# Kernel tuning notes

Hardware: AMD Instinct MI355X
Metric: run time of the kernel (lower is better)

The kernel has to match this reference:

```python
import jax, jax.numpy as jnp
import numpy as np
from jax import lax

E, C, N = 3, 2, 2048          # edge types, channels, nodes (= nb_items)
B, T = 64, 50                 # batch, max_seq_length
W_IN = 256; W_OUT = 256; U = 512  # gcn in/out, rnn_units


def setup_inputs() -> dict:
    key = jax.random.key(0)
    ks = jax.random.split(key, 16)
    # sparse-ish adjacency stored densely (coalesce/spspmm equivalents are dense ops)
    A = jnp.where(jax.random.uniform(ks[0], (E, N, N)) < 0.01,
                  jax.random.uniform(ks[1], (E, N, N)), 0.0)
    X = jax.random.normal(ks[2], (N, W_IN)) * 0.1
    seqs = (jax.random.uniform(ks[3], (B, T, N)) < 0.005).astype(jnp.float32)  # multi-hot baskets
    seq_len = jax.random.randint(ks[4], (B,), 1, T + 1)
    h0 = jnp.zeros((B, U), jnp.float32)
    c0 = jnp.zeros((B, U), jnp.float32)
    # GTConv weights: init constant 1 (softmax -> uniform filter)
    gt_w1 = jnp.ones((C, E), jnp.float32)
    gt_w2 = jnp.ones((C, E), jnp.float32)
    gt_w3 = jnp.ones((C, E), jnp.float32)
    s_in = 1.0 / np.sqrt(W_IN)
    gcn_W = jax.random.normal(ks[5], (W_IN, W_OUT)) * s_in
    gcn_b = jnp.zeros((W_OUT,), jnp.float32)
    lin1_W = jax.random.normal(ks[6], (C * W_OUT, W_OUT)) * (1.0 / np.sqrt(C * W_OUT))
    lin1_b = jnp.zeros((W_OUT,), jnp.float32)
    s_u = 1.0 / np.sqrt(U)
    lstm_Wih = jax.random.normal(ks[7], (4 * U, W_OUT)) * s_u
    lstm_Whh = jax.random.normal(ks[8], (4 * U, U)) * s_u
    lstm_bih = jnp.zeros((4 * U,), jnp.float32)
    lstm_bhh = jnp.zeros((4 * U,), jnp.float32)
    score_W = jax.random.normal(ks[9], (N, U)) * s_u
    return {"A": A, "X": X, "seqs": seqs, "seq_len": seq_len, "h0": h0, "c0": c0,
            "gt_w1": gt_w1, "gt_w2": gt_w2, "gt_w3": gt_w3,
            "gcn_W": gcn_W, "gcn_b": gcn_b, "lin1_W": lin1_W, "lin1_b": lin1_b,
            "lstm_Wih": lstm_Wih, "lstm_Whh": lstm_Whh,
            "lstm_bih": lstm_bih, "lstm_bhh": lstm_bhh, "score_W": score_W}


def _gtconv(A, w):
    # filter = softmax over edge types; per-channel convex combine of adjacencies
    f = jax.nn.softmax(w, axis=1)            # [C,E]
    return jnp.einsum('ce,enm->cnm', f, A)   # [C,N,N]


def _col_normalize(H):
    # remove self loops; deg = scatter_add over col; value *= deg_col^-1 (no_grad deg)
    H = H * (1.0 - jnp.eye(N, dtype=H.dtype))
    deg = H.sum(axis=1)                      # [C,N] per-column degree
    dinv = lax.stop_gradient(jnp.where(deg > 0, 1.0 / deg, 0.0))
    return H * dinv[:, None, :]


def _gcn(M, X, W, b):
    # PyG GCNConv: add self loops, sym-normalize by col/row degree, aggregate at target
    M1 = M + jnp.eye(N, dtype=M.dtype)
    deg = M1.sum(axis=0)                     # scatter over col
    dis = jnp.where(deg > 0, lax.rsqrt(deg), 0.0)
    Ahat = dis[:, None] * M1 * dis[None, :]
    return Ahat.T @ (X @ W) + b              # out[target] = sum_src norm * x[src]


def reference(A, X, seqs, seq_len, h0, c0, gt_w1, gt_w2, gt_w3,
              gcn_W, gcn_b, lin1_W, lin1_b,
              lstm_Wih, lstm_Whh, lstm_bih, lstm_bhh, score_W):
    # --- GT layers: H = conv1(A) @ conv2(A), then H = norm(H) @ conv(A) ---
    HA = _gtconv(A, gt_w1)
    HB = _gtconv(A, gt_w2)
    H = jnp.einsum('cnk,ckm->cnm', HA, HB)          # spspmm per channel
    Hn = _col_normalize(H)
    HB2 = _gtconv(A, gt_w3)
    H = jnp.einsum('cnk,ckm->cnm', Hn, HB2)
    # --- GCN per channel, relu, concat, linear1 ---
    feats = [jax.nn.relu(_gcn(H[i], X, gcn_W, gcn_b)) for i in range(C)]
    X_ = jnp.concatenate(feats, axis=1) @ lin1_W + lin1_b   # [N, W_OUT]
    # --- basket max-pooling over items in each basket (empty -> zeros) ---
    def pool_step(_, mask_t):                # mask_t: [B,N]
        masked = jnp.where(mask_t[:, :, None] > 0, X_[None, :, :], -jnp.inf)
        pooled = masked.max(axis=1)          # [B, W_OUT]
        has = mask_t.sum(axis=1) > 0
        return None, jnp.where(has[:, None], pooled, 0.0)
    _, bs = lax.scan(pool_step, None, jnp.swapaxes(seqs, 0, 1))  # [T,B,W_OUT]
    # --- single-layer LSTM (PyTorch gate order i,f,g,o) ---
    def lstm_step(carry, x_t):
        h, c = carry
        g = x_t @ lstm_Wih.T + h @ lstm_Whh.T + lstm_bih + lstm_bhh
        i, f, gg, o = jnp.split(g, 4, axis=-1)
        c = jax.nn.sigmoid(f) * c + jax.nn.sigmoid(i) * jnp.tanh(gg)
        h = jax.nn.sigmoid(o) * jnp.tanh(c)
        return (h, c), h
    _, outs = lax.scan(lstm_step, (h0, c0), bs)      # [T,B,U]
    lstm_out = jnp.swapaxes(outs, 0, 1)              # [B,T,U]
    actual = lstm_out[jnp.arange(B), seq_len - 1]    # [B,U] last valid step
    return jax.nn.sigmoid(actual @ score_W.T)        # [B,N]
```

## Files before the change

kernel.cpp:

```cpp
#include <hip/hip_runtime.h>
#include <stdint.h>

#define E_ 3
#define C_ 2
#define N_ 2048
#define B_ 64
#define T_ 50
#define WIN_ 256
#define WOUT_ 256
#define U_ 512
#define BT_ (B_*T_)
#define BTP_ 3328

typedef unsigned short u16;
typedef unsigned int u32;
typedef __bf16 bf16x8 __attribute__((ext_vector_type(8)));
typedef float f32x4 __attribute__((ext_vector_type(4)));

#define NN_ (2048LL*2048LL)

__device__ __forceinline__ float bf2f(u16 u){
  u32 x = ((u32)u) << 16; return __builtin_bit_cast(float, x);
}
__device__ __forceinline__ u16 f2bf(float f){
  u32 x = __builtin_bit_cast(u32, f);
  u32 r = (x + 0x7fffu + ((x >> 16) & 1u)) >> 16;
  return (u16)r;
}

__device__ __forceinline__ void gload16(const u16* g, u16* l){
  __builtin_amdgcn_global_load_lds((const __attribute__((address_space(1))) u32*)g,
                                   (__attribute__((address_space(3))) u32*)l, 16, 0, 0);
}

__global__ void k_prep0(const float* __restrict__ w1, const float* __restrict__ w2,
                        const float* __restrict__ w3, float* __restrict__ filt,
                        const float* __restrict__ bih, const float* __restrict__ bhh,
                        float* __restrict__ bsum, u32* __restrict__ flagv){
  const int i = blockIdx.x*256 + threadIdx.x;
  bsum[i] = bih[i] + bhh[i];
  flagv[i] = 0;
  if(blockIdx.x==0 && threadIdx.x < 3*C_){
    const int t = threadIdx.x;
    const int fi = t / C_, c = t % C_;
    const float* w = (fi==0) ? w1 : ((fi==1) ? w2 : w3);
    float v[E_]; float mx = -3.4e38f;
    for(int e=0;e<E_;e++){ v[e] = w[c*E_+e]; mx = fmaxf(mx, v[e]); }
    float s = 0.f;
    for(int e=0;e<E_;e++){ v[e] = expf(v[e]-mx); s += v[e]; }
    for(int e=0;e<E_;e++) filt[(fi*C_+c)*E_ + e] = v[e]/s;
  }
}

__global__ void k_combineAll(const float* __restrict__ A, const float* __restrict__ filt,
                             u16* __restrict__ HA, u16* __restrict__ HBt){
  __shared__ float te[3][32][33];
  const int ti = blockIdx.x, tj = blockIdx.y;
  const int x = threadIdx.x, y0 = threadIdx.y;
  #pragma unroll
  for(int i=0;i<4;i++){
    const int y = y0 + i*8;
    const long base = (long)(tj*32+y)*N_ + ti*32 + x;
    const float a0 = A[0*NN_+base], a1 = A[1*NN_+base], a2 = A[2*NN_+base];
    te[0][y][x]=a0; te[1][y][x]=a1; te[2][y][x]=a2;
    #pragma unroll
    for(int c=0;c<C_;c++)
      HA[c*NN_ + base] = f2bf(filt[c*E_]*a0 + filt[c*E_+1]*a1 + filt[c*E_+2]*a2);
  }
  __syncthreads();
  #pragma unroll
  for(int i=0;i<4;i++){
    const int y = y0 + i*8;
    const long ob = (long)(ti*32+y)*N_ + tj*32 + x;
    const float a0=te[0][x][y], a1=te[1][x][y], a2=te[2][x][y];
    #pragma unroll
    for(int c=0;c<C_;c++)
      HBt[c*NN_+ob] = f2bf(filt[(C_+c)*E_]*a0 + filt[(C_+c)*E_+1]*a1 + filt[(C_+c)*E_+2]*a2);
  }
}

__global__ void k_combineT2(const float* __restrict__ A, const float* __restrict__ f,
                            u16* __restrict__ outp){
  __shared__ float te[3][32][33];
  const int ti = blockIdx.x, tj = blockIdx.y;
  const int x = threadIdx.x, y0 = threadIdx.y;
  #pragma unroll
  for(int i=0;i<4;i++){
    const int y = y0 + i*8;
    const long base = (long)(tj*32+y)*N_ + ti*32 + x;
    te[0][y][x]=A[0*NN_+base]; te[1][y][x]=A[1*NN_+base]; te[2][y][x]=A[2*NN_+base];
  }
  __syncthreads();
  #pragma unroll
  for(int i=0;i<4;i++){
    const int y = y0 + i*8;
    const long ob = (long)(ti*32+y)*N_ + tj*32 + x;
    const float a0=te[0][x][y], a1=te[1][x][y], a2=te[2][x][y];
    #pragma unroll
    for(int c=0;c<C_;c++)
      outp[c*NN_+ob] = f2bf(f[c*E_]*a0 + f[c*E_+1]*a1 + f[c*E_+2]*a2);
  }
}

template<int MODE>
__global__ __launch_bounds__(256) void gemm_bt(
    const u16* __restrict__ Ag, const u16* __restrict__ Bg, void* __restrict__ Cg,
    int K, int ldc, long sA, long sB, long sC,
    const float* __restrict__ disv, int sDis, const float* __restrict__ bias)
{
  __shared__ u16 At[128*32];
  __shared__ u16 Bt[128*32];
  const int tid = threadIdx.x;
  const int w = tid >> 6, l = tid & 63;
  const int z = blockIdx.z;
  const u16* Ab = Ag + (long)z*sA;
  const u16* Bb = Bg + (long)z*sB;
  const int rowBase = blockIdx.y*128;
  const int colBase = blockIdx.x*128;

  f32x4 acc[4][4];
  #pragma unroll
  for(int i=0;i<4;i++)
    #pragma unroll
    for(int j=0;j<4;j++)
      acc[i][j] = f32x4{0.f,0.f,0.f,0.f};

  const int wr = w >> 1, wc = w & 1;
  const int arow0 = (w*2+0)*16 + (l>>2);
  const int arow1 = (w*2+1)*16 + (l>>2);
  const int kc = (((l&3) ^ ((l>>2)&3)))*8;
  const int frow = l & 15;
  const int fkc = l >> 4;

  const int nk = K >> 5;
  for(int kt=0; kt<nk; ++kt){
    const int k0 = kt << 5;
    gload16(Ab + (long)(rowBase+arow0)*K + k0 + kc, &At[(w*2+0)*512]);
    gload16(Ab + (long)(rowBase+arow1)*K + k0 + kc, &At[(w*2+1)*512]);
    gload16(Bb + (long)(colBase+arow0)*K + k0 + kc, &Bt[(w*2+0)*512]);
    gload16(Bb + (long)(colBase+arow1)*K + k0 + kc, &Bt[(w*2+1)*512]);
    __syncthreads();
    bf16x8 af[4], bfv[4];
    #pragma unroll
    for(int m=0;m<4;m++){
      const int rr = wr*64 + m*16 + frow;
      af[m] = *(const bf16x8*)&At[rr*32 + ((fkc ^ (rr&3))<<3)];
    }
    #pragma unroll
    for(int n=0;n<4;n++){
      const int rr = wc*64 + n*16 + frow;
      bfv[n] = *(const bf16x8*)&Bt[rr*32 + ((fkc ^ (rr&3))<<3)];
    }
    #pragma unroll
    for(int m=0;m<4;m++)
      #pragma unroll
      for(int n=0;n<4;n++)
        acc[m][n] = __builtin_amdgcn_mfma_f32_16x16x32_bf16(af[m], bfv[n], acc[m][n], 0, 0, 0);
    __syncthreads();
  }

  #pragma unroll
  for(int m=0;m<4;m++){
    const int row0 = rowBase + wr*64 + m*16 + (l>>4)*4;
    #pragma unroll
    for(int n=0;n<4;n++){
      const int col = colBase + wc*64 + n*16 + (l&15);
      #pragma unroll
      for(int r=0;r<4;r++){
        const float v = acc[m][n][r];
        if(MODE==1){
          ((u16*)Cg)[z*sC + (long)(row0+r)*ldc + col] = f2bf(v);
        } else if(MODE==2){
          float o = disv[z*(long)sDis + row0 + r]*v + bias[col];
          o = o > 0.f ? o : 0.f;
          ((u16*)Cg)[z*sC + (long)(row0+r)*ldc + col] = f2bf(o);
        } else if(MODE==3){
          ((float*)Cg)[z*sC + (long)(row0+r)*ldc + col] = v + bias[col];
        } else if(MODE==4){
          const int row = row0 + r;
          if(row < BT_){
            const int bb = row/50, tt = row - bb*50;
            const int gq = col >> 9, ugg = col & 511;
            ((float*)Cg)[((((long)tt*4 + (bb>>4))*512 + ugg)*16 + (bb&15))*4 + gq] = v + bias[col];
          }
        }
      }
    }
  }
}

__global__ void k_degpart(const u16* __restrict__ H, float* __restrict__ partial){
  const int c = blockIdx.z;
  const int col = blockIdx.x*256 + threadIdx.x;
  const int r0 = blockIdx.y*128;
  const u16* Hc = H + c*NN_;
  float s = 0.f;
  #pragma unroll 4
  for(int r=0;r<128;r++) s += bf2f(Hc[(long)(r0+r)*N_ + col]);
  partial[((long)c*16 + blockIdx.y)*N_ + col] = s;
}

__global__ void k_dinv(const u16* __restrict__ H, const float* __restrict__ partial,
                       float* __restrict__ dinvb){
  const int i = blockIdx.x*256 + threadIdx.x;
  const int c = i >> 11, m = i & (N_-1);
  float s = 0.f;
  #pragma unroll
  for(int p=0;p<16;p++) s += partial[((long)c*16 + p)*N_ + m];
  s -= bf2f(H[c*NN_ + (long)m*N_ + m]);
  dinvb[i] = s > 0.f ? 1.f/s : 0.f;
}

__global__ void k_colscale(u16* __restrict__ H, const float* __restrict__ dinvb){
  const long i = (long)blockIdx.x*256 + threadIdx.x;
  const int c = blockIdx.y;
  const int j = (int)(i >> 11), ii = (int)(i & (N_-1));
  const long idx = c*NN_ + i;
  const float v = (j==ii) ? 0.f : bf2f(H[idx])*dinvb[c*N_ + ii];
  H[idx] = f2bf(v);
}

__global__ void k_gcnprep(const u16* __restrict__ H2t, float* __restrict__ disv){
  const int c = blockIdx.y, j = blockIdx.x;
  const u16* r = H2t + (c*(long)N_ + j)*N_;
  float s = 0.f;
  for(int i=threadIdx.x;i<N_;i+=256) s += bf2f(r[i]);
  __shared__ float red[256];
  red[threadIdx.x] = s;
  __syncthreads();
  for(int st=128; st>0; st>>=1){
    if(threadIdx.x < st) red[threadIdx.x] += red[threadIdx.x+st];
    __syncthreads();
  }
  if(threadIdx.x==0){
    const float deg = red[0] + 1.f;
    disv[c*N_ + j] = deg > 0.f ? rsqrtf(deg) : 0.f;
  }
}

__global__ void k_pd(const u16* __restrict__ H2t, const float* __restrict__ disv,
                     u16* __restrict__ Pd){
  const long i = (long)blockIdx.x*256 + threadIdx.x;
  const int c = blockIdx.y;
  const int j = (int)(i >> 11);
  const int ii = (int)(i & (N_-1));
  const long idx = c*NN_ + i;
  const float v = bf2f(H2t[idx]) + (ii==j ? 1.f : 0.f);
  Pd[idx] = f2bf(v*disv[c*N_ + ii]);
}

__global__ void k_transpose3(const float* __restrict__ gcnW, u16* __restrict__ Wt,
                             const float* __restrict__ lin1W, u16* __restrict__ l1Wt,
                             const float* __restrict__ scoreW, u16* __restrict__ sWt){
  const float* in; u16* out; int R, Cc;
  if(blockIdx.z==0){ in=gcnW;  out=Wt;   R=WIN_;     Cc=WOUT_; }
  else if(blockIdx.z==1){ in=lin1W; out=l1Wt; R=C_*WOUT_; Cc=WOUT_; }
  else { in=scoreW; out=sWt; R=N_; Cc=U_; }
  const int ti = blockIdx.x, tj = blockIdx.y;
  if(ti >= (Cc>>5) || tj >= (R>>5)) return;
  __shared__ float tt[32][33];
  const int x = threadIdx.x, y0 = threadIdx.y;
  #pragma unroll
  for(int i=0;i<4;i++){
    const int y = y0 + i*8;
    tt[y][x] = in[(long)(tj*32+y)*Cc + ti*32 + x];
  }
  __syncthreads();
  #pragma unroll
  for(int i=0;i<4;i++){
    const int y = y0 + i*8;
    out[(long)(ti*32+y)*R + tj*32 + x] = f2bf(tt[x][y]);
  }
}

__global__ void k_cast2(const float* __restrict__ X, u16* __restrict__ Xbf,
                        const float* __restrict__ Wih, u16* __restrict__ Wihbf){
  const long i = (long)blockIdx.x*256 + threadIdx.x;
  if(i < (long)N_*WIN_) Xbf[i] = f2bf(X[i]);
  else { const long j = i - (long)N_*WIN_; Wihbf[j] = f2bf(Wih[j]); }
}

__global__ void k_pool(const float* __restrict__ seqs, const float* __restrict__ X_,
                       u16* __restrict__ bs){
  const int t = blockIdx.x, b = blockIdx.y;
  const int f = threadIdx.x;
  if(t >= T_){
    bs[(long)(BT_ + b*2 + (t-T_))*WOUT_ + f] = 0;
    return;
  }
  const float* mask = seqs + ((long)b*T_ + t)*N_;
  __shared__ int list[N_];
  __shared__ int cnt;
  if(f==0) cnt = 0;
  __syncthreads();
  for(int n0=f; n0<N_; n0+=256){
    if(mask[n0] > 0.f){
      int p = atomicAdd(&cnt, 1);
      list[p] = n0;
    }
  }
  __syncthreads();
  const int m = cnt;
  float mx = -3.4e38f;
  for(int i=0;i<m;i++)
    mx = fmaxf(mx, X_[(long)list[i]*WOUT_ + f]);
  bs[((long)b*T_ + t)*WOUT_ + f] = f2bf(m>0 ? mx : 0.f);
}

__global__ void k_packWhh3(const float* __restrict__ Whh, u16* __restrict__ P){
  const long idx = (long)blockIdx.x*256 + threadIdx.x;
  const int e  = (int)(idx & 7);
  const int kk = (int)((idx >> 3) & 15);
  const int l  = (int)((idx >> 7) & 63);
  const int w  = (int)((idx >> 13) & 7);
  const int s  = (int)(idx >> 16);
  const int lr = w*16 + (l & 15);
  const int gam = lr & 3, ui = lr >> 2;
  const int grow = gam*512 + s*32 + ui;
  const int k = kk*32 + (l >> 4)*8 + e;
  P[idx] = f2bf(Whh[(long)grow*512 + k]);
}

__global__ void k_hinit(const float* __restrict__ h0, u16* __restrict__ Hglob){
  const int idx = blockIdx.x*256 + threadIdx.x;
  const int b = idx >> 9, u = idx & 511;
  const int grp = b >> 4, bl = b & 15;
  Hglob[grp*16384 + (bl << 9) + (u ^ ((bl & 7) << 3))] = f2bf(h0[idx]);
}

__global__ __launch_bounds__(512) void k_lstm_all(
    const u16* __restrict__ WhhP, const float* __restrict__ Gq,
    const float* __restrict__ c0v, const int* __restrict__ seqlen,
    u16* __restrict__ Hglob, u32* __restrict__ flagv, float* __restrict__ act)
{
  __shared__ u16 Hl[16*512];
  const int tid = threadIdx.x;
  const int w = tid >> 6, l = tid & 63;
  const int grp = blockIdx.x & 3, s = blockIdx.x >> 2;
  const int fr = l & 15, hi = l >> 4;

  bf16x8 wreg[16];
  const u16* wp = WhhP + (((long)s*8 + w)*64 + l)*128;
  #pragma unroll
  for(int kk=0; kk<16; ++kk)
    wreg[kk] = *(const bf16x8*)&wp[kk*8];

  const int ui = w*4 + hi;
  const int ug = s*32 + ui;
  const int bl = fr;
  const int bg = grp*16 + bl;
  float cst = c0v[bg*U_ + ug];
  const int sl = seqlen[bg] - 1;
  u16* Hbase = Hglob + grp*16384;
  const int hswz = (bl & 7) << 3;
  const int fi = (grp*16 + fr)*32;
  const long gqbase = (((long)grp*512 + ug)*16 + bl)*4;

  float4 gq_nxt = *(const float4*)&Gq[gqbase];

  for(int t=0; t<T_; ++t){
    const float4 gq = gq_nxt;
    const u16* Hin = Hbase + (t & 1)*8192;
    #pragma unroll
    for(int r=0; r<2; ++r)
      gload16(Hin + (r*8 + w)*512 + l*8, &Hl[(r*8 + w)*512]);
    __syncthreads();

    f32x4 acc = f32x4{0.f,0.f,0.f,0.f};
    #pragma unroll
    for(int kk=0; kk<16; ++kk){
      const int ke = kk*32 + hi*8;
      bf16x8 bb = *(const bf16x8*)&Hl[(bl << 9) + (ke ^ hswz)];
      acc = __builtin_amdgcn_mfma_f32_16x16x32_bf16(wreg[kk], bb, acc, 0, 0, 0);
    }

    if(t+1 < T_)
      gq_nxt = *(const float4*)&Gq[(long)(t+1)*(4*2048*16) + gqbase];

    const float a0 = acc[0] + gq.x;
    const float a1 = acc[1] + gq.y;
    const float a2 = acc[2] + gq.z;
    const float a3 = acc[3] + gq.w;
    const float ig = 1.f/(1.f + expf(-a0));
    const float fg = 1.f/(1.f + expf(-a1));
    const float gg = tanhf(a2);
    const float og = 1.f/(1.f + expf(-a3));
    cst = fg*cst + ig*gg;
    const float h = og*tanhf(cst);
    u16* Hout = Hbase + ((t+1) & 1)*8192;
    Hout[(bl << 9) + (ug ^ hswz)] = f2bf(h);
    if(sl == t) act[bg*U_ + ug] = h;

    if(t == T_-1) break;
    __syncthreads();
    if(tid == 0)
      __hip_atomic_store(&flagv[(grp*16 + s)*32], (u32)(t+1),
                         __ATOMIC_RELEASE, __HIP_MEMORY_SCOPE_AGENT);
    if(w == 0){
      while(__hip_atomic_load(&flagv[fi], __ATOMIC_ACQUIRE,
                              __HIP_MEMORY_SCOPE_AGENT) <= (u32)t){
        __builtin_amdgcn_s_sleep(1);
      }
    }
    __syncthreads();
  }
}

__global__ void k_score(const float* __restrict__ actual, const u16* __restrict__ sWt,
                        float* __restrict__ out){
  const int n = blockIdx.x*256 + threadIdx.x;
  const int b = blockIdx.y;
  const float* ab = actual + (long)b*U_;
  float s = 0.f;
  for(int uu=0; uu<U_; uu++) s += ab[uu]*bf2f(sWt[(long)uu*N_ + n]);
  out[(long)b*N_ + n] = 1.f/(1.f + expf(-s));
}

extern "C" void kernel_launch(void* const* d_in, const int* in_sizes, int n_in,
                              void* d_out, int out_size, void* d_ws, size_t ws_size,
                              hipStream_t stream){
  (void)in_sizes; (void)n_in; (void)out_size; (void)ws_size;
  const float* A      = (const float*)d_in[0];
  const float* X      = (const float*)d_in[1];
  const float* seqs   = (const float*)d_in[2];
  const int*   seqlen = (const int*)d_in[3];
  const float* h0     = (const float*)d_in[4];
  const float* c0     = (const float*)d_in[5];
  const float* gtw1   = (const float*)d_in[6];
  const float* gtw2   = (const float*)d_in[7];
  const float* gtw3   = (const float*)d_in[8];
  const float* gcnW   = (const float*)d_in[9];
  const float* gcnB   = (const float*)d_in[10];
  const float* lin1W  = (const float*)d_in[11];
  const float* lin1B  = (const float*)d_in[12];
  const float* Wih    = (const float*)d_in[13];
  const float* Whh    = (const float*)d_in[14];
  const float* bihp   = (const float*)d_in[15];
  const float* bhhp   = (const float*)d_in[16];
  const float* scoreW = (const float*)d_in[17];

  char* ws = (char*)d_ws;
  u16* buf0 = (u16*)(ws + 0);
  u16* buf1 = (u16*)(ws + 16777216);
  u16* buf2 = (u16*)(ws + 33554432);
  char* S0  = ws + 50331648;
  float* filt  = (float*)(S0 + 0);
  float* disv  = (float*)(S0 + 1024);
  u16*  Wt     = (u16*) (S0 + 17408);
  u16*  XWt    = (u16*) (S0 + 148480);
  u16*  catb   = (u16*) (S0 + 1197056);
  u16*  l1Wt   = (u16*) (S0 + 3294208);
  float* Xo    = (float*)(S0 + 3556352);
  u16*  bs     = (u16*) (S0 + 5653504);
  float* act   = (float*)(S0 + 7357440);
  u16*  sWt    = (u16*) (S0 + 7488512);
  u16*  WhhB   = (u16*) (S0 + 9585664);
  u16*  Xbf    = (u16*) (S0 + 11682816);
  u16*  Wihbf  = (u16*) (S0 + 12731392);
  float* bsum  = (float*)(S0 + 13779968);
  u16*  Hglob  = (u16*) (S0 + 13788160);
  u32*  flagv  = (u32*) (S0 + 13919232);
  float* degp  = (float*)(S0 + 14050304);
  float* dinvb = (float*)(S0 + 14312448);
  u16* HA   = buf0;
  u16* HBt  = buf1;
  u16* Hb   = buf2;
  u16* HB2t = buf0;
  u16* H2t  = buf1;
  u16* Pd   = buf1;
  float* Gq = (float*)ws;

  k_prep0<<<dim3(8), 256, 0, stream>>>(gtw1, gtw2, gtw3, filt, bihp, bhhp, bsum, flagv);
  k_combineAll<<<dim3(N_/32, N_/32), dim3(32,8), 0, stream>>>(A, filt, HA, HBt);
  k_transpose3<<<dim3(16, 64, 3), dim3(32,8), 0, stream>>>(gcnW, Wt, lin1W, l1Wt, scoreW, sWt);
  k_cast2<<<dim3(4096), 256, 0, stream>>>(X, Xbf, Wih, Wihbf);
  gemm_bt<1><<<dim3(16,16,C_), 256, 0, stream>>>(HA, HBt, Hb, N_, N_, NN_, NN_, NN_, nullptr, 0, nullptr);
  k_degpart<<<dim3(8, 16, C_), 256, 0, stream>>>(Hb, degp);
  k_dinv<<<dim3(16), 256, 0, stream>>>(Hb, degp, dinvb);
  k_colscale<<<dim3(NN_/256, C_), 256, 0, stream>>>(Hb, dinvb);
  k_combineT2<<<dim3(N_/32, N_/32), dim3(32,8), 0, stream>>>(A, filt + 2*C_*E_, HB2t);
  gemm_bt<1><<<dim3(16,16,C_), 256, 0, stream>>>(HB2t, Hb, H2t, N_, N_, NN_, NN_, NN_, nullptr, 0, nullptr);
  k_gcnprep<<<dim3(N_, C_), 256, 0, stream>>>(H2t, disv);
  k_pd<<<dim3(NN_/256, C_), 256, 0, stream>>>(H2t, disv, Pd);
  gemm_bt<1><<<dim3(N_/128, WOUT_/128, 1), 256, 0, stream>>>(Wt, Xbf, XWt, WIN_, N_, 0, 0, 0, nullptr, 0, nullptr);
  gemm_bt<2><<<dim3(WOUT_/128, N_/128, C_), 256, 0, stream>>>(Pd, XWt, catb, N_, C_*WOUT_, NN_, 0, WOUT_, disv, N_, gcnB);
  gemm_bt<3><<<dim3(WOUT_/128, N_/128, 1), 256, 0, stream>>>(catb, l1Wt, Xo, C_*WOUT_, WOUT_, 0, 0, 0, nullptr, 0, lin1B);
  k_pool<<<dim3(52, B_), 256, 0, stream>>>(seqs, Xo, bs);
  gemm_bt<4><<<dim3((4*U_)/128, BTP_/128, 1), 256, 0, stream>>>(bs, Wihbf, Gq, WOUT_, 0, 0, 0, 0, nullptr, 0, bsum);
  k_packWhh3<<<dim3(4096), 256, 0, stream>>>(Whh, WhhB);
  k_hinit<<<dim3(128), 256, 0, stream>>>(h0, Hglob);
  k_lstm_all<<<dim3(64), 512, 0, stream>>>(WhhB, Gq, c0, seqlen, Hglob, flagv, act);
  k_score<<<dim3(N_/256, B_), 256, 0, stream>>>(act, sWt, (float*)d_out);
}
```

Before: 576.5 us.

## Fuse degree normalization into GEMM epilogue and run score projection as MFMA GEMM

Result: faster. 562.0 us (-2.5%).

```diff
diff --git a/kernel.cpp b/kernel.cpp
--- a/kernel.cpp
+++ b/kernel.cpp
@@ -180,9 +180,17 @@
           const int row = row0 + r;
           if(row < BT_){
             const int bb = row/50, tt = row - bb*50;
-            const int gq = col >> 9, ugg = col & 511;
-            ((float*)Cg)[((((long)tt*4 + (bb>>4))*512 + ugg)*16 + (bb&15))*4 + gq] = v + bias[col];
+            const int gate = col >> 9, ugg = col & 511;
+            ((float*)Cg)[((((long)tt*4 + (bb>>4))*512 + ugg)*16 + (bb&15))*4 + gate] = v + bias[col];
           }
+        } else if(MODE==5){
+          const int row = row0 + r;
+          const float o = (v + (row==col ? 1.f : 0.f)) * disv[z*(long)sDis + col];
+          ((u16*)Cg)[z*sC + (long)row*ldc + col] = f2bf(o);
+        } else if(MODE==6){
+          const int row = row0 + r;
+          if(row < B_)
+            ((float*)Cg)[(long)row*ldc + col] = 1.f/(1.f + expf(-v));
         }
       }
     }
@@ -220,11 +228,14 @@
   H[idx] = f2bf(v);
 }
 
-__global__ void k_gcnprep(const u16* __restrict__ H2t, float* __restrict__ disv){
+__global__ void k_dis(const u16* __restrict__ HB2t, const float* __restrict__ dinvb,
+                      float* __restrict__ disv){
   const int c = blockIdx.y, j = blockIdx.x;
-  const u16* r = H2t + (c*(long)N_ + j)*N_;
+  const u16* r = HB2t + (c*(long)N_ + j)*N_;
+  const float* dv = dinvb + c*N_;
   float s = 0.f;
-  for(int i=threadIdx.x;i<N_;i+=256) s += bf2f(r[i]);
+  for(int i=threadIdx.x;i<N_;i+=256)
+    if(dv[i] > 0.f) s += bf2f(r[i]);
   __shared__ float red[256];
   red[threadIdx.x] = s;
   __syncthreads();
@@ -238,24 +249,11 @@
   }
 }
 
-__global__ void k_pd(const u16* __restrict__ H2t, const float* __restrict__ disv,
-                     u16* __restrict__ Pd){
-  const long i = (long)blockIdx.x*256 + threadIdx.x;
-  const int c = blockIdx.y;
-  const int j = (int)(i >> 11);
-  const int ii = (int)(i & (N_-1));
-  const long idx = c*NN_ + i;
-  const float v = bf2f(H2t[idx]) + (ii==j ? 1.f : 0.f);
-  Pd[idx] = f2bf(v*disv[c*N_ + ii]);
-}
-
 __global__ void k_transpose3(const float* __restrict__ gcnW, u16* __restrict__ Wt,
-                             const float* __restrict__ lin1W, u16* __restrict__ l1Wt,
-                             const float* __restrict__ scoreW, u16* __restrict__ sWt){
+                             const float* __restrict__ lin1W, u16* __restrict__ l1Wt){
   const float* in; u16* out; int R, Cc;
   if(blockIdx.z==0){ in=gcnW;  out=Wt;   R=WIN_;     Cc=WOUT_; }
-  else if(blockIdx.z==1){ in=lin1W; out=l1Wt; R=C_*WOUT_; Cc=WOUT_; }
-  else { in=scoreW; out=sWt; R=N_; Cc=U_; }
+  else { in=lin1W; out=l1Wt; R=C_*WOUT_; Cc=WOUT_; }
   const int ti = blockIdx.x, tj = blockIdx.y;
   if(ti >= (Cc>>5) || tj >= (R>>5)) return;
   __shared__ float tt[32][33];
@@ -273,11 +271,16 @@
   }
 }
 
-__global__ void k_cast2(const float* __restrict__ X, u16* __restrict__ Xbf,
-                        const float* __restrict__ Wih, u16* __restrict__ Wihbf){
+__global__ void k_cast3(const float* __restrict__ X, u16* __restrict__ Xbf,
+                        const float* __restrict__ Wih, u16* __restrict__ Wihbf,
+                        const float* __restrict__ scoreW, u16* __restrict__ sWbf){
   const long i = (long)blockIdx.x*256 + threadIdx.x;
   if(i < (long)N_*WIN_) Xbf[i] = f2bf(X[i]);
-  else { const long j = i - (long)N_*WIN_; Wihbf[j] = f2bf(Wih[j]); }
+  else if(i < (long)N_*WIN_ + 4*U_*WOUT_){
+    const long j = i - (long)N_*WIN_; Wihbf[j] = f2bf(Wih[j]);
+  } else {
+    const long j = i - (long)N_*WIN_ - 4*U_*WOUT_; sWbf[j] = f2bf(scoreW[j]);
+  }
 }
 
 __global__ void k_pool(const float* __restrict__ seqs, const float* __restrict__ X_,
@@ -331,7 +334,7 @@
 __global__ __launch_bounds__(512) void k_lstm_all(
     const u16* __restrict__ WhhP, const float* __restrict__ Gq,
     const float* __restrict__ c0v, const int* __restrict__ seqlen,
-    u16* __restrict__ Hglob, u32* __restrict__ flagv, float* __restrict__ act)
+    u16* __restrict__ Hglob, u32* __restrict__ flagv, u16* __restrict__ act)
 {
   __shared__ u16 Hl[16*512];
   const int tid = threadIdx.x;
@@ -345,8 +348,7 @@
   for(int kk=0; kk<16; ++kk)
     wreg[kk] = *(const bf16x8*)&wp[kk*8];
 
-  const int ui = w*4 + hi;
-  const int ug = s*32 + ui;
+  const int ug = s*32 + w*4 + hi;
   const int bl = fr;
   const int bg = grp*16 + bl;
   float cst = c0v[bg*U_ + ug];
@@ -355,7 +357,6 @@
   const int hswz = (bl & 7) << 3;
   const int fi = (grp*16 + fr)*32;
   const long gqbase = (((long)grp*512 + ug)*16 + bl)*4;
-
   float4 gq_nxt = *(const float4*)&Gq[gqbase];
 
   for(int t=0; t<T_; ++t){
@@ -389,7 +390,7 @@
     const float h = og*tanhf(cst);
     u16* Hout = Hbase + ((t+1) & 1)*8192;
     Hout[(bl << 9) + (ug ^ hswz)] = f2bf(h);
-    if(sl == t) act[bg*U_ + ug] = h;
+    if(sl == t) act[bg*U_ + ug] = f2bf(h);
 
     if(t == T_-1) break;
     __syncthreads();
@@ -404,16 +405,6 @@
     }
     __syncthreads();
   }
-}
-
-__global__ void k_score(const float* __restrict__ actual, const u16* __restrict__ sWt,
-                        float* __restrict__ out){
-  const int n = blockIdx.x*256 + threadIdx.x;
-  const int b = blockIdx.y;
-  const float* ab = actual + (long)b*U_;
-  float s = 0.f;
-  for(int uu=0; uu<U_; uu++) s += ab[uu]*bf2f(sWt[(long)uu*N_ + n]);
-  out[(long)b*N_ + n] = 1.f/(1.f + expf(-s));
 }
 
 extern "C" void kernel_launch(void* const* d_in, const int* in_sizes, int n_in,
@@ -452,8 +443,8 @@
   u16*  l1Wt   = (u16*) (S0 + 3294208);
   float* Xo    = (float*)(S0 + 3556352);
   u16*  bs     = (u16*) (S0 + 5653504);
-  float* act   = (float*)(S0 + 7357440);
-  u16*  sWt    = (u16*) (S0 + 7488512);
+  u16*  act    = (u16*) (S0 + 7357440);
+  u16*  sWbf   = (u16*) (S0 + 7488512);
   u16*  WhhB   = (u16*) (S0 + 9585664);
   u16*  Xbf    = (u16*) (S0 + 11682816);
   u16*  Wihbf  = (u16*) (S0 + 12731392);
@@ -466,22 +457,20 @@
   u16* HBt  = buf1;
   u16* Hb   = buf2;
   u16* HB2t = buf0;
-  u16* H2t  = buf1;
   u16* Pd   = buf1;
   float* Gq = (float*)ws;
 
   k_prep0<<<dim3(8), 256, 0, stream>>>(gtw1, gtw2, gtw3, filt, bihp, bhhp, bsum, flagv);
   k_combineAll<<<dim3(N_/32, N_/32), dim3(32,8), 0, stream>>>(A, filt, HA, HBt);
-  k_transpose3<<<dim3(16, 64, 3), dim3(32,8), 0, stream>>>(gcnW, Wt, lin1W, l1Wt, scoreW, sWt);
-  k_cast2<<<dim3(4096), 256, 0, stream>>>(X, Xbf, Wih, Wihbf);
+  k_transpose3<<<dim3(16, 64, 2), dim3(32,8), 0, stream>>>(gcnW, Wt, lin1W, l1Wt);
+  k_cast3<<<dim3(8192), 256, 0, stream>>>(X, Xbf, Wih, Wihbf, scoreW, sWbf);
   gemm_bt<1><<<dim3(16,16,C_), 256, 0, stream>>>(HA, HBt, Hb, N_, N_, NN_, NN_, NN_, nullptr, 0, nullptr);
   k_degpart<<<dim3(8, 16, C_), 256, 0, stream>>>(Hb, degp);
   k_dinv<<<dim3(16), 256, 0, stream>>>(Hb, degp, dinvb);
   k_colscale<<<dim3(NN_/256, C_), 256, 0, stream>>>(Hb, dinvb);
   k_combineT2<<<dim3(N_/32, N_/32), dim3(32,8), 0, stream>>>(A, filt + 2*C_*E_, HB2t);
-  gemm_bt<1><<<dim3(16,16,C_), 256, 0, stream>>>(HB2t, Hb, H2t, N_, N_, NN_, NN_, NN_, nullptr, 0, nullptr);
-  k_gcnprep<<<dim3(N_, C_), 256, 0, stream>>>(H2t, disv);
-  k_pd<<<dim3(NN_/256, C_), 256, 0, stream>>>(H2t, disv, Pd);
+  k_dis<<<dim3(N_, C_), 256, 0, stream>>>(HB2t, dinvb, disv);
+  gemm_bt<5><<<dim3(16,16,C_), 256, 0, stream>>>(HB2t, Hb, Pd, N_, N_, NN_, NN_, NN_, disv, N_, nullptr);
   gemm_bt<1><<<dim3(N_/128, WOUT_/128, 1), 256, 0, stream>>>(Wt, Xbf, XWt, WIN_, N_, 0, 0, 0, nullptr, 0, nullptr);
   gemm_bt<2><<<dim3(WOUT_/128, N_/128, C_), 256, 0, stream>>>(Pd, XWt, catb, N_, C_*WOUT_, NN_, 0, WOUT_, disv, N_, gcnB);
   gemm_bt<3><<<dim3(WOUT_/128, N_/128, 1), 256, 0, stream>>>(catb, l1Wt, Xo, C_*WOUT_, WOUT_, 0, 0, 0, nullptr, 0, lin1B);
@@ -490,5 +479,5 @@
   k_packWhh3<<<dim3(4096), 256, 0, stream>>>(Whh, WhhB);
   k_hinit<<<dim3(128), 256, 0, stream>>>(h0, Hglob);
   k_lstm_all<<<dim3(64), 512, 0, stream>>>(WhhB, Gq, c0, seqlen, Hglob, flagv, act);
-  k_score<<<dim3(N_/256, B_), 256, 0, stream>>>(act, sWt, (float*)d_out);
-}
+  gemm_bt<6><<<dim3(N_/128, 1, 1), 256, 0, stream>>>(act, sWbf, (float*)d_out, U_, N_, 0, 0, 0, nullptr, 0, nullptr);
+}
```
